# Performance work log

Measured on AMD Instinct MI355X. Metric: run time of the kernel, lower is better.

The kernel has to match this reference:

```python
import jax, jax.numpy as jnp
import numpy as np

INPUT_SIZE = 2048
HIDDEN_SIZE = 2048
BATCH = 4096


def setup_inputs() -> dict:
    key = jax.random.key(0)
    ks = jax.random.split(key, 16)
    s_in = 1.0 / np.sqrt(INPUT_SIZE)
    s_h = 1.0 / np.sqrt(HIDDEN_SIZE)
    d = {
        "x": jax.random.normal(ks[0], (BATCH, INPUT_SIZE), jnp.float32),
        "h": jax.random.normal(ks[1], (BATCH, HIDDEN_SIZE), jnp.float32),
        "c": jax.random.normal(ks[2], (BATCH, HIDDEN_SIZE), jnp.float32),
    }
    # input-side weights [H, I] and biases (torch nn.Linear layout)
    for i, g in enumerate(["f", "i", "c", "o"]):
        d[f"W{g}x"] = jax.random.uniform(ks[3 + i], (HIDDEN_SIZE, INPUT_SIZE), jnp.float32, -s_in, s_in)
        d[f"b{g}x"] = jax.random.uniform(ks[7 + i], (HIDDEN_SIZE,), jnp.float32, -s_in, s_in)
        d[f"W{g}h"] = jax.random.uniform(ks[11 + i], (HIDDEN_SIZE, HIDDEN_SIZE), jnp.float32, -s_h, s_h)
    return d


def reference(x, h, c, Wfx, bfx, Wfh, Wix, bix, Wih, Wcx, bcx, Wch, Wox, box, Woh):
    # gate pre-activations: x @ W*x.T + b + h @ W*h.T
    f = jax.nn.relu(x @ Wfx.T + bfx + h @ Wfh.T)
    i = jax.nn.relu(x @ Wix.T + bix + h @ Wih.T)
    o = jax.nn.relu(x @ Wox.T + box + h @ Woh.T)
    c_tilde = jnp.tanh(x @ Wcx.T + bcx + h @ Wch.T)
    c_new = f * c + i * c_tilde
    h_new = o * jnp.tanh(c_new)
    return (h_new, c_new)
```

## Files before the change

### kernel.cpp

```cpp
#include <hip/hip_runtime.h>
#include <hip/hip_bf16.h>


#define HID 2048
#define BATCH_N 4096
#define KTOT 4096
#define BK 64

typedef __attribute__((ext_vector_type(4))) float f32x4;
typedef __attribute__((ext_vector_type(8))) short bf16x8;

__device__ __forceinline__ short f2bf(float f) {
    union { float f; unsigned u; } v; v.f = f;
    unsigned r = v.u + 0x7FFFu + ((v.u >> 16) & 1u);
    return (short)(r >> 16);
}

__device__ __forceinline__ float fast_tanh(float v) {
    float e = __expf(2.0f * v);
    return 1.0f - 2.0f / (e + 1.0f);
}

__device__ __forceinline__ void gload_lds16(const short* g, short* l) {
    __builtin_amdgcn_global_load_lds(
        (const __attribute__((address_space(1))) unsigned int*)g,
        (__attribute__((address_space(3))) unsigned int*)l, 16, 0, 0);
}

struct CastParams {
    const float* x; const float* h;
    const float* Wx[4]; const float* Wh[4];
    short* A; short* B;
};

__global__ __launch_bounds__(256) void precast_kernel(CastParams q) {
    const long A_CH = (long)BATCH_N * (KTOT / 8);
    const long B_CH = 4L * HID * (KTOT / 8);
    const long total = A_CH + B_CH;
    for (long idx = (long)blockIdx.x * 256 + threadIdx.x; idx < total;
         idx += (long)gridDim.x * 256) {
        const float* src; short* dst; int row, k;
        if (idx < A_CH) {
            row = (int)(idx >> 9);
            k = (int)(idx & 511) << 3;
            src = (k < HID) ? &q.x[(size_t)row * HID + k]
                            : &q.h[(size_t)row * HID + (k - HID)];
            dst = &q.A[(size_t)row * KTOT];
        } else {
            long r = idx - A_CH;
            int g = (int)(r >> 20);
            int rem = (int)(r & ((1 << 20) - 1));
            row = rem >> 9;
            k = (rem & 511) << 3;
            src = (k < HID) ? &q.Wx[g][(size_t)row * HID + k]
                            : &q.Wh[g][(size_t)row * HID + (k - HID)];
            dst = &q.B[((size_t)g * HID + row) * KTOT];
        }
        float4 v0 = *(const float4*)src;
        float4 v1 = *(const float4*)(src + 4);
        int col = (k & ~63) | ((k & 63) ^ ((row & 7) << 3));
        bf16x8 s;
        s[0] = f2bf(v0.x); s[1] = f2bf(v0.y); s[2] = f2bf(v0.z); s[3] = f2bf(v0.w);
        s[4] = f2bf(v1.x); s[5] = f2bf(v1.y); s[6] = f2bf(v1.z); s[7] = f2bf(v1.w);
        *(bf16x8*)&dst[col] = s;
    }
}

struct GemmParams {
    const short* A; const short* B;
    const float* bx[4];
    const float* c;
    float* oh; float* oc;
};

__global__ __launch_bounds__(512, 2) void gemm_lstm_8ph(GemmParams p) {
    __shared__ short sA[2][16384];
    __shared__ short sB[2][16384];

    const int t = threadIdx.x;
    const int wave = t >> 6;
    const int lane = t & 63;
    const int wr = wave >> 1;
    const int wc = wave & 1;
    const int lr = lane & 15;
    const int lk = (lane >> 4) * 8;
    const int sw = (lane & 7) << 3;
    const int koff0 = lk ^ sw;
    const int koff1 = (32 + lk) ^ sw;

    const int bm = blockIdx.x * 256;
    const int bn = blockIdx.y * 64;

    const int aOff = (wr * 64 + lr) * 64;
    const int bOff = (wc * 32 + lr) * 64;

    const short* aSrc = p.A + (size_t)(bm + (t >> 3)) * KTOT + (t & 7) * 8;
    const short* bSrc = p.B + (size_t)(bn + (t >> 3)) * KTOT + (t & 7) * 8;
    const int ldsT = t * 8;

    f32x4 acc[4][4][2];
    #pragma unroll
    for (int g = 0; g < 4; ++g)
        #pragma unroll
        for (int m = 0; m < 4; ++m)
            #pragma unroll
            for (int n = 0; n < 2; ++n)
                acc[g][m][n] = (f32x4){0.f, 0.f, 0.f, 0.f};

    bf16x8 a[4][2];
    bf16x8 b[2][2];

#define STAGE_A(bf, u, kp) gload_lds16(aSrc + (size_t)(u) * 64 * KTOT + (kp), \
                                       &sA[bf][(u) * 4096 + ldsT])
#define STAGE_B(bf, g, kp) gload_lds16(bSrc + (size_t)(g) * HID * KTOT + (kp), \
                                       &sB[bf][(g) * 4096 + ldsT])
#define READ_A(bf) do { _Pragma("unroll") for (int m = 0; m < 4; ++m) { \
        a[m][0] = *(const bf16x8*)&sA[bf][aOff + m * 1024 + koff0]; \
        a[m][1] = *(const bf16x8*)&sA[bf][aOff + m * 1024 + koff1]; } } while (0)
#define READ_B(bf, g) do { _Pragma("unroll") for (int n = 0; n < 2; ++n) { \
        b[n][0] = *(const bf16x8*)&sB[bf][(g) * 4096 + bOff + n * 1024 + koff0]; \
        b[n][1] = *(const bf16x8*)&sB[bf][(g) * 4096 + bOff + n * 1024 + koff1]; } } while (0)
#define MFMA_G(g) do { __builtin_amdgcn_s_setprio(1); \
        _Pragma("unroll") for (int kk = 0; kk < 2; ++kk) \
        _Pragma("unroll") for (int n = 0; n < 2; ++n) \
        _Pragma("unroll") for (int m = 0; m < 4; ++m) \
            acc[g][m][n] = __builtin_amdgcn_mfma_f32_16x16x32_bf16( \
                a[m][kk], b[n][kk], acc[g][m][n], 0, 0, 0); \
        __builtin_amdgcn_s_setprio(0); } while (0)
#define BAR() __builtin_amdgcn_s_barrier()
#define VMCNT6() asm volatile("s_waitcnt vmcnt(6)" ::: "memory")

    STAGE_A(0, 0, 0); STAGE_A(0, 1, 0); STAGE_A(0, 2, 0); STAGE_A(0, 3, 0);
    STAGE_B(0, 0, 0); STAGE_B(0, 1, 0); STAGE_B(0, 2, 0); STAGE_B(0, 3, 0);
    STAGE_A(1, 0, BK); STAGE_A(1, 1, BK); STAGE_A(1, 2, BK); STAGE_A(1, 3, BK);
    STAGE_B(1, 0, BK); STAGE_B(1, 1, BK);
    VMCNT6();
    BAR();

    for (int it = 0; it < KTOT / (2 * BK); ++it) {
        const int kc1 = ((2 * it + 1) * BK) & (KTOT - 1);
        const int kc2 = ((2 * it + 2) * BK) & (KTOT - 1);
        const int kc3 = ((2 * it + 3) * BK) & (KTOT - 1);

        READ_A(0); READ_B(0, 0);
        STAGE_B(1, 2, kc1); STAGE_B(1, 3, kc1);
        BAR(); MFMA_G(0); BAR();
        READ_B(0, 1);
        STAGE_A(0, 0, kc2); STAGE_A(0, 1, kc2);
        BAR(); MFMA_G(1); BAR();
        READ_B(0, 2);
        STAGE_A(0, 2, kc2); STAGE_A(0, 3, kc2);
        BAR(); MFMA_G(2); BAR();
        READ_B(0, 3);
        STAGE_B(0, 0, kc2); STAGE_B(0, 1, kc2);
        VMCNT6();
        BAR(); MFMA_G(3); BAR();
        READ_A(1); READ_B(1, 0);
        STAGE_B(0, 2, kc2); STAGE_B(0, 3, kc2);
        BAR(); MFMA_G(0); BAR();
        READ_B(1, 1);
        STAGE_A(1, 0, kc3); STAGE_A(1, 1, kc3);
        BAR(); MFMA_G(1); BAR();
        READ_B(1, 2);
        STAGE_A(1, 2, kc3); STAGE_A(1, 3, kc3);
        BAR(); MFMA_G(2); BAR();
        READ_B(1, 3);
        STAGE_B(1, 0, kc3); STAGE_B(1, 1, kc3);
        VMCNT6();
        BAR(); MFMA_G(3); BAR();
    }
    asm volatile("s_waitcnt vmcnt(0)" ::: "memory");

    float bias[4][2];
    #pragma unroll
    for (int g = 0; g < 4; ++g)
        #pragma unroll
        for (int n = 0; n < 2; ++n)
            bias[g][n] = p.bx[g][bn + wc * 32 + n * 16 + lr];

    #pragma unroll
    for (int m = 0; m < 4; ++m) {
        int rbase = bm + wr * 64 + m * 16 + (lane >> 4) * 4;
        #pragma unroll
        for (int r = 0; r < 4; ++r) {
            int row = rbase + r;
            #pragma unroll
            for (int n = 0; n < 2; ++n) {
                int col = bn + wc * 32 + n * 16 + lr;
                float pf = acc[0][m][n][r] + bias[0][n];
                float pi = acc[1][m][n][r] + bias[1][n];
                float pc = acc[2][m][n][r] + bias[2][n];
                float po = acc[3][m][n][r] + bias[3][n];
                float fg = fmaxf(pf, 0.f);
                float ig = fmaxf(pi, 0.f);
                float og = fmaxf(po, 0.f);
                float ct = fast_tanh(pc);
                float cv = p.c[(size_t)row * HID + col];
                float cn = fg * cv + ig * ct;
                float hn = og * fast_tanh(cn);
                p.oh[(size_t)row * HID + col] = hn;
                p.oc[(size_t)row * HID + col] = cn;
            }
        }
    }
#undef STAGE_A
#undef STAGE_B
#undef READ_A
#undef READ_B
#undef MFMA_G
#undef BAR
#undef VMCNT6
}

struct Params {
    const float* x; const float* h; const float* c;
    const float* Wx[4]; const float* Wh[4]; const float* bx[4];
    float* oh; float* oc;
};

__global__ __launch_bounds__(256, 2) void relulstm_fallback(Params p) {
    __shared__ short sA[128 * 64];
    __shared__ short sB[4][64 * 64];
    const int t = threadIdx.x;
    const int bm = blockIdx.x * 128;
    const int bn = blockIdx.y * 64;
    const int wave = t >> 6;
    const int lane = t & 63;
    const int wm = (wave >> 1) * 64;
    const int wn = (wave & 1) * 32;
    const int lr = lane & 15;
    const int lk = (lane >> 4) * 8;

    f32x4 acc[4][4][2];
    #pragma unroll
    for (int g = 0; g < 4; ++g)
        #pragma unroll
        for (int m = 0; m < 4; ++m)
            #pragma unroll
            for (int n = 0; n < 2; ++n)
                acc[g][m][n] = (f32x4){0.f, 0.f, 0.f, 0.f};

    for (int k0 = 0; k0 < 2 * HID; k0 += BK) {
        const bool xpart = (k0 < HID);
        const int kb = k0 & (HID - 1);
        const float* __restrict__ srcA = xpart ? p.x : p.h;
        #pragma unroll
        for (int i2 = 0; i2 < 8; ++i2) {
            int cidx = t + i2 * 256;
            int row = cidx >> 4;
            int kc = cidx & 15;
            float4 v = *(const float4*)&srcA[(size_t)(bm + row) * HID + kb + kc * 4];
            int idx = row * BK + ((kc * 4) ^ ((row & 7) << 3));
            short4 s;
            s.x = f2bf(v.x); s.y = f2bf(v.y); s.z = f2bf(v.z); s.w = f2bf(v.w);
            *(short4*)&sA[idx] = s;
        }
        #pragma unroll
        for (int i2 = 0; i2 < 16; ++i2) {
            const int g = i2 >> 2;
            int rem = t + (i2 & 3) * 256;
            int row = rem >> 4;
            int kc = rem & 15;
            const float* __restrict__ srcB = xpart ? p.Wx[g] : p.Wh[g];
            float4 v = *(const float4*)&srcB[(size_t)(bn + row) * HID + kb + kc * 4];
            int idx = row * BK + ((kc * 4) ^ ((row & 7) << 3));
            short4 s;
            s.x = f2bf(v.x); s.y = f2bf(v.y); s.z = f2bf(v.z); s.w = f2bf(v.w);
            *(short4*)&sB[g][idx] = s;
        }
        __syncthreads();
        #pragma unroll
        for (int kk = 0; kk < 2; ++kk) {
            bf16x8 a[4];
            #pragma unroll
            for (int m = 0; m < 4; ++m) {
                int row = wm + m * 16 + lr;
                int kidx = (kk * 32 + lk) ^ ((row & 7) << 3);
                a[m] = *(const bf16x8*)&sA[row * BK + kidx];
            }
            #pragma unroll
            for (int g = 0; g < 4; ++g) {
                #pragma unroll
                for (int n = 0; n < 2; ++n) {
                    int brow = wn + n * 16 + lr;
                    int kidx = (kk * 32 + lk) ^ ((brow & 7) << 3);
                    bf16x8 b = *(const bf16x8*)&sB[g][brow * BK + kidx];
                    #pragma unroll
                    for (int m = 0; m < 4; ++m)
                        acc[g][m][n] = __builtin_amdgcn_mfma_f32_16x16x32_bf16(
                            a[m], b, acc[g][m][n], 0, 0, 0);
                }
            }
        }
        __syncthreads();
    }

    float bias[4][2];
    #pragma unroll
    for (int g = 0; g < 4; ++g)
        #pragma unroll
        for (int n = 0; n < 2; ++n)
            bias[g][n] = p.bx[g][bn + wn + n * 16 + lr];

    #pragma unroll
    for (int m = 0; m < 4; ++m) {
        int rbase = bm + wm + m * 16 + (lane >> 4) * 4;
        #pragma unroll
        for (int r = 0; r < 4; ++r) {
            int row = rbase + r;
            #pragma unroll
            for (int n = 0; n < 2; ++n) {
                int col = bn + wn + n * 16 + lr;
                float pf = acc[0][m][n][r] + bias[0][n];
                float pi = acc[1][m][n][r] + bias[1][n];
                float pc = acc[2][m][n][r] + bias[2][n];
                float po = acc[3][m][n][r] + bias[3][n];
                float fg = fmaxf(pf, 0.f);
                float ig = fmaxf(pi, 0.f);
                float og = fmaxf(po, 0.f);
                float ct = fast_tanh(pc);
                float cv = p.c[(size_t)row * HID + col];
                float cn = fg * cv + ig * ct;
                float hn = og * fast_tanh(cn);
                p.oh[(size_t)row * HID + col] = hn;
                p.oc[(size_t)row * HID + col] = cn;
            }
        }
    }
}

extern "C" void kernel_launch(void* const* d_in, const int* in_sizes, int n_in,
                              void* d_out, int out_size, void* d_ws, size_t ws_size,
                              hipStream_t stream) {
    (void)in_sizes; (void)n_in; (void)out_size;
    const size_t A_BYTES = (size_t)BATCH_N * KTOT * 2;
    const size_t B_BYTES = (size_t)4 * HID * KTOT * 2;

    if (ws_size >= A_BYTES + B_BYTES) {
        short* A = (short*)d_ws;
        short* B = A + (size_t)BATCH_N * KTOT;

        CastParams q;
        q.x = (const float*)d_in[0];
        q.h = (const float*)d_in[1];
        for (int g = 0; g < 4; ++g) {
            q.Wx[g] = (const float*)d_in[3 + 3 * g];
            q.Wh[g] = (const float*)d_in[5 + 3 * g];
        }
        q.A = A; q.B = B;
        precast_kernel<<<2048, 256, 0, stream>>>(q);

        GemmParams p;
        p.A = A; p.B = B;
        p.c = (const float*)d_in[2];
        for (int g = 0; g < 4; ++g) p.bx[g] = (const float*)d_in[4 + 3 * g];
        p.oh = (float*)d_out;
        p.oc = (float*)d_out + (size_t)BATCH_N * HID;
        dim3 grid(BATCH_N / 256, HID / 64);
        gemm_lstm_8ph<<<grid, 512, 0, stream>>>(p);
    } else {
        Params p;
        p.x = (const float*)d_in[0];
        p.h = (const float*)d_in[1];
        p.c = (const float*)d_in[2];
        for (int g = 0; g < 4; ++g) {
            p.Wx[g] = (const float*)d_in[3 + 3 * g];
            p.bx[g] = (const float*)d_in[4 + 3 * g];
            p.Wh[g] = (const float*)d_in[5 + 3 * g];
        }
        p.oh = (float*)d_out;
        p.oc = (float*)d_out + (size_t)BATCH_N * HID;
        dim3 grid(BATCH_N / 128, HID / 64);
        relulstm_fallback<<<grid, 256, 0, stream>>>(p);
    }
}
```

Measured before the change: 317.4 us.

## Switch to 32x32x16 MFMA tiles and remap blocks for L2 locality

Replaces the 16x16x32 bf16 MFMA tiling with 32x32x16 MFMAs, so each wave issues fewer, larger matrix instructions and issues fewer LDS reads per FLOP. The LDS fragment offsets and the fused LSTM epilogue's row/column mapping are rewritten to match the 32x32 accumulator layout. It also flattens the grid to 1D with an XCD-aware block swizzle to improve cache reuse, and adds an lgkmcnt wait before the first MFMA group. The changed epilogue store pattern and new wait placement could affect memory efficiency or overlap.

```diff
diff --git a/kernel.cpp b/kernel.cpp
--- a/kernel.cpp
+++ b/kernel.cpp
@@ -8,6 +8,7 @@
 #define BK 64
 
 typedef __attribute__((ext_vector_type(4))) float f32x4;
+typedef __attribute__((ext_vector_type(16))) float f32x16;
 typedef __attribute__((ext_vector_type(8))) short bf16x8;
 
 __device__ __forceinline__ short f2bf(float f) {
@@ -82,53 +83,56 @@
     const int lane = t & 63;
     const int wr = wave >> 1;
     const int wc = wave & 1;
-    const int lr = lane & 15;
-    const int lk = (lane >> 4) * 8;
-    const int sw = (lane & 7) << 3;
-    const int koff0 = lk ^ sw;
-    const int koff1 = (32 + lk) ^ sw;
-
-    const int bm = blockIdx.x * 256;
-    const int bn = blockIdx.y * 64;
-
-    const int aOff = (wr * 64 + lr) * 64;
-    const int bOff = (wc * 32 + lr) * 64;
+    const int l31 = lane & 31;
+    const int kb_ = (lane >> 5) * 8;
+    const int sw = (l31 & 7) << 3;
+
+    int kx[4];
+    #pragma unroll
+    for (int ks = 0; ks < 4; ++ks) kx[ks] = (ks * 16 + kb_) ^ sw;
+
+    const int b0 = blockIdx.x;
+    const int nb = ((b0 & 7) << 6) | (b0 >> 3);
+    const int bm = (nb & 15) * 256;
+    const int bn = (nb >> 4) * 64;
+
+    const int aOff = (wr * 64 + l31) * 64;
+    const int bOff = (wc * 32 + l31) * 64;
 
     const short* aSrc = p.A + (size_t)(bm + (t >> 3)) * KTOT + (t & 7) * 8;
     const short* bSrc = p.B + (size_t)(bn + (t >> 3)) * KTOT + (t & 7) * 8;
     const int ldsT = t * 8;
 
-    f32x4 acc[4][4][2];
+    f32x16 acc[4][2];
     #pragma unroll
     for (int g = 0; g < 4; ++g)
         #pragma unroll
-        for (int m = 0; m < 4; ++m)
-            #pragma unroll
-            for (int n = 0; n < 2; ++n)
-                acc[g][m][n] = (f32x4){0.f, 0.f, 0.f, 0.f};
-
-    bf16x8 a[4][2];
-    bf16x8 b[2][2];
+        for (int m = 0; m < 2; ++m)
+            #pragma unroll
+            for (int r = 0; r < 16; ++r)
+                acc[g][m][r] = 0.f;
+
+    bf16x8 a[2][4];
+    bf16x8 b[4];
 
 #define STAGE_A(bf, u, kp) gload_lds16(aSrc + (size_t)(u) * 64 * KTOT + (kp), \
                                        &sA[bf][(u) * 4096 + ldsT])
 #define STAGE_B(bf, g, kp) gload_lds16(bSrc + (size_t)(g) * HID * KTOT + (kp), \
                                        &sB[bf][(g) * 4096 + ldsT])
-#define READ_A(bf) do { _Pragma("unroll") for (int m = 0; m < 4; ++m) { \
-        a[m][0] = *(const bf16x8*)&sA[bf][aOff + m * 1024 + koff0]; \
-        a[m][1] = *(const bf16x8*)&sA[bf][aOff + m * 1024 + koff1]; } } while (0)
-#define READ_B(bf, g) do { _Pragma("unroll") for (int n = 0; n < 2; ++n) { \
-        b[n][0] = *(const bf16x8*)&sB[bf][(g) * 4096 + bOff + n * 1024 + koff0]; \
-        b[n][1] = *(const bf16x8*)&sB[bf][(g) * 4096 + bOff + n * 1024 + koff1]; } } while (0)
+#define READ_A(bf) do { _Pragma("unroll") for (int m = 0; m < 2; ++m) \
+        _Pragma("unroll") for (int ks = 0; ks < 4; ++ks) \
+            a[m][ks] = *(const bf16x8*)&sA[bf][aOff + m * 2048 + kx[ks]]; } while (0)
+#define READ_B(bf, g) do { _Pragma("unroll") for (int ks = 0; ks < 4; ++ks) \
+            b[ks] = *(const bf16x8*)&sB[bf][(g) * 4096 + bOff + kx[ks]]; } while (0)
 #define MFMA_G(g) do { __builtin_amdgcn_s_setprio(1); \
-        _Pragma("unroll") for (int kk = 0; kk < 2; ++kk) \
-        _Pragma("unroll") for (int n = 0; n < 2; ++n) \
-        _Pragma("unroll") for (int m = 0; m < 4; ++m) \
-            acc[g][m][n] = __builtin_amdgcn_mfma_f32_16x16x32_bf16( \
-                a[m][kk], b[n][kk], acc[g][m][n], 0, 0, 0); \
+        _Pragma("unroll") for (int ks = 0; ks < 4; ++ks) \
+        _Pragma("unroll") for (int m = 0; m < 2; ++m) \
+            acc[g][m] = __builtin_amdgcn_mfma_f32_32x32x16_bf16( \
+                a[m][ks], b[ks], acc[g][m], 0, 0, 0); \
         __builtin_amdgcn_s_setprio(0); } while (0)
 #define BAR() __builtin_amdgcn_s_barrier()
 #define VMCNT6() asm volatile("s_waitcnt vmcnt(6)" ::: "memory")
+#define LGKM8() asm volatile("s_waitcnt lgkmcnt(8)" ::: "memory")
 
     STAGE_A(0, 0, 0); STAGE_A(0, 1, 0); STAGE_A(0, 2, 0); STAGE_A(0, 3, 0);
     STAGE_B(0, 0, 0); STAGE_B(0, 1, 0); STAGE_B(0, 2, 0); STAGE_B(0, 3, 0);
@@ -144,6 +148,7 @@
 
         READ_A(0); READ_B(0, 0);
         STAGE_B(1, 2, kc1); STAGE_B(1, 3, kc1);
+        LGKM8();
         BAR(); MFMA_G(0); BAR();
         READ_B(0, 1);
         STAGE_A(0, 0, kc2); STAGE_A(0, 1, kc2);
@@ -157,6 +162,7 @@
         BAR(); MFMA_G(3); BAR();
         READ_A(1); READ_B(1, 0);
         STAGE_B(0, 2, kc2); STAGE_B(0, 3, kc2);
+        LGKM8();
         BAR(); MFMA_G(0); BAR();
         READ_B(1, 1);
         STAGE_A(1, 0, kc3); STAGE_A(1, 1, kc3);
@@ -171,36 +177,29 @@
     }
     asm volatile("s_waitcnt vmcnt(0)" ::: "memory");
 
-    float bias[4][2];
-    #pragma unroll
-    for (int g = 0; g < 4; ++g)
-        #pragma unroll
-        for (int n = 0; n < 2; ++n)
-            bias[g][n] = p.bx[g][bn + wc * 32 + n * 16 + lr];
-
-    #pragma unroll
-    for (int m = 0; m < 4; ++m) {
-        int rbase = bm + wr * 64 + m * 16 + (lane >> 4) * 4;
-        #pragma unroll
-        for (int r = 0; r < 4; ++r) {
-            int row = rbase + r;
-            #pragma unroll
-            for (int n = 0; n < 2; ++n) {
-                int col = bn + wc * 32 + n * 16 + lr;
-                float pf = acc[0][m][n][r] + bias[0][n];
-                float pi = acc[1][m][n][r] + bias[1][n];
-                float pc = acc[2][m][n][r] + bias[2][n];
-                float po = acc[3][m][n][r] + bias[3][n];
-                float fg = fmaxf(pf, 0.f);
-                float ig = fmaxf(pi, 0.f);
-                float og = fmaxf(po, 0.f);
-                float ct = fast_tanh(pc);
-                float cv = p.c[(size_t)row * HID + col];
-                float cn = fg * cv + ig * ct;
-                float hn = og * fast_tanh(cn);
-                p.oh[(size_t)row * HID + col] = hn;
-                p.oc[(size_t)row * HID + col] = cn;
-            }
+    const int col = bn + wc * 32 + l31;
+    float bias[4];
+    #pragma unroll
+    for (int g = 0; g < 4; ++g) bias[g] = p.bx[g][col];
+
+    #pragma unroll
+    for (int m = 0; m < 2; ++m) {
+        #pragma unroll
+        for (int r = 0; r < 16; ++r) {
+            int row = bm + wr * 64 + m * 32 + (r & 3) + 8 * (r >> 2) + 4 * (lane >> 5);
+            float pf = acc[0][m][r] + bias[0];
+            float pi = acc[1][m][r] + bias[1];
+            float pc = acc[2][m][r] + bias[2];
+            float po = acc[3][m][r] + bias[3];
+            float fg = fmaxf(pf, 0.f);
+            float ig = fmaxf(pi, 0.f);
+            float og = fmaxf(po, 0.f);
+            float ct = fast_tanh(pc);
+            float cv = p.c[(size_t)row * HID + col];
+            float cn = fg * cv + ig * ct;
+            float hn = og * fast_tanh(cn);
+            p.oh[(size_t)row * HID + col] = hn;
+            p.oc[(size_t)row * HID + col] = cn;
         }
     }
 #undef STAGE_A
@@ -210,6 +209,7 @@
 #undef MFMA_G
 #undef BAR
 #undef VMCNT6
+#undef LGKM8
 }
 
 struct Params {
@@ -356,8 +356,7 @@
         for (int g = 0; g < 4; ++g) p.bx[g] = (const float*)d_in[4 + 3 * g];
         p.oh = (float*)d_out;
         p.oc = (float*)d_out + (size_t)BATCH_N * HID;
-        dim3 grid(BATCH_N / 256, HID / 64);
-        gemm_lstm_8ph<<<grid, 512, 0, stream>>>(p);
+        gemm_lstm_8ph<<<dim3(512), 512, 0, stream>>>(p);
     } else {
         Params p;
         p.x = (const float*)d_in[0];
```

Result: slower. 352.2 us (+10.9%).

## Double-buffer LDS fragments in registers and halve barriers per GEMM phase

Applied to the files above, without the earlier changes.

Splits the A/B register fragments into two ping-pong sets, so the next gate's B fragment (and the next K-chunk's A fragment) is read from LDS while the current MFMA group runs. Each phase now ends with a single barrier plus a scheduling barrier instead of bracketing every MFMA group with two barriers. The vmcnt wait moves earlier and drops to 4, so the other buffer is complete before it is read ahead. This aims to hide LDS read latency and cut barrier stalls, at the cost of extra VGPRs for the second fragment set and a stricter scheduling order.

```diff
diff --git a/kernel.cpp b/kernel.cpp
--- a/kernel.cpp
+++ b/kernel.cpp
@@ -73,7 +73,7 @@
     float* oh; float* oc;
 };
 
-__global__ __launch_bounds__(512, 2) void gemm_lstm_8ph(GemmParams p) {
+__global__ __launch_bounds__(512, 2) void gemm_lstm_pipe(GemmParams p) {
     __shared__ short sA[2][16384];
     __shared__ short sB[2][16384];
 
@@ -107,67 +107,81 @@
             for (int n = 0; n < 2; ++n)
                 acc[g][m][n] = (f32x4){0.f, 0.f, 0.f, 0.f};
 
-    bf16x8 a[4][2];
-    bf16x8 b[2][2];
+    bf16x8 aX[4][2], aY[4][2];
+    bf16x8 bX[2][2], bY[2][2];
 
 #define STAGE_A(bf, u, kp) gload_lds16(aSrc + (size_t)(u) * 64 * KTOT + (kp), \
                                        &sA[bf][(u) * 4096 + ldsT])
 #define STAGE_B(bf, g, kp) gload_lds16(bSrc + (size_t)(g) * HID * KTOT + (kp), \
                                        &sB[bf][(g) * 4096 + ldsT])
-#define READ_A(bf) do { _Pragma("unroll") for (int m = 0; m < 4; ++m) { \
-        a[m][0] = *(const bf16x8*)&sA[bf][aOff + m * 1024 + koff0]; \
-        a[m][1] = *(const bf16x8*)&sA[bf][aOff + m * 1024 + koff1]; } } while (0)
-#define READ_B(bf, g) do { _Pragma("unroll") for (int n = 0; n < 2; ++n) { \
-        b[n][0] = *(const bf16x8*)&sB[bf][(g) * 4096 + bOff + n * 1024 + koff0]; \
-        b[n][1] = *(const bf16x8*)&sB[bf][(g) * 4096 + bOff + n * 1024 + koff1]; } } while (0)
-#define MFMA_G(g) do { __builtin_amdgcn_s_setprio(1); \
+#define READ_A_TO(dst, bf) do { _Pragma("unroll") for (int m = 0; m < 4; ++m) { \
+        dst[m][0] = *(const bf16x8*)&sA[bf][aOff + m * 1024 + koff0]; \
+        dst[m][1] = *(const bf16x8*)&sA[bf][aOff + m * 1024 + koff1]; } } while (0)
+#define READ_B_TO(dst, bf, g) do { _Pragma("unroll") for (int n = 0; n < 2; ++n) { \
+        dst[n][0] = *(const bf16x8*)&sB[bf][(g) * 4096 + bOff + n * 1024 + koff0]; \
+        dst[n][1] = *(const bf16x8*)&sB[bf][(g) * 4096 + bOff + n * 1024 + koff1]; } } while (0)
+#define MFMA_G(g, aS, bS) do { __builtin_amdgcn_s_setprio(1); \
         _Pragma("unroll") for (int kk = 0; kk < 2; ++kk) \
         _Pragma("unroll") for (int n = 0; n < 2; ++n) \
         _Pragma("unroll") for (int m = 0; m < 4; ++m) \
             acc[g][m][n] = __builtin_amdgcn_mfma_f32_16x16x32_bf16( \
-                a[m][kk], b[n][kk], acc[g][m][n], 0, 0, 0); \
+                aS[m][kk], bS[n][kk], acc[g][m][n], 0, 0, 0); \
         __builtin_amdgcn_s_setprio(0); } while (0)
-#define BAR() __builtin_amdgcn_s_barrier()
-#define VMCNT6() asm volatile("s_waitcnt vmcnt(6)" ::: "memory")
+#define ENDW() do { __builtin_amdgcn_s_barrier(); \
+                    __builtin_amdgcn_sched_barrier(0); } while (0)
+#define VMCNT(n) asm volatile("s_waitcnt vmcnt(" #n ")" ::: "memory")
 
     STAGE_A(0, 0, 0); STAGE_A(0, 1, 0); STAGE_A(0, 2, 0); STAGE_A(0, 3, 0);
     STAGE_B(0, 0, 0); STAGE_B(0, 1, 0); STAGE_B(0, 2, 0); STAGE_B(0, 3, 0);
     STAGE_A(1, 0, BK); STAGE_A(1, 1, BK); STAGE_A(1, 2, BK); STAGE_A(1, 3, BK);
     STAGE_B(1, 0, BK); STAGE_B(1, 1, BK);
-    VMCNT6();
-    BAR();
+    VMCNT(6);
+    __builtin_amdgcn_s_barrier();
+    READ_A_TO(aX, 0);
+    READ_B_TO(bX, 0, 0);
+    ENDW();
 
     for (int it = 0; it < KTOT / (2 * BK); ++it) {
         const int kc1 = ((2 * it + 1) * BK) & (KTOT - 1);
         const int kc2 = ((2 * it + 2) * BK) & (KTOT - 1);
         const int kc3 = ((2 * it + 3) * BK) & (KTOT - 1);
 
-        READ_A(0); READ_B(0, 0);
+        READ_B_TO(bY, 0, 1);
         STAGE_B(1, 2, kc1); STAGE_B(1, 3, kc1);
-        BAR(); MFMA_G(0); BAR();
-        READ_B(0, 1);
+        MFMA_G(0, aX, bX);
+        ENDW();
+        READ_B_TO(bX, 0, 2);
         STAGE_A(0, 0, kc2); STAGE_A(0, 1, kc2);
-        BAR(); MFMA_G(1); BAR();
-        READ_B(0, 2);
+        MFMA_G(1, aX, bY);
+        ENDW();
+        READ_B_TO(bY, 0, 3);
         STAGE_A(0, 2, kc2); STAGE_A(0, 3, kc2);
-        BAR(); MFMA_G(2); BAR();
-        READ_B(0, 3);
+        MFMA_G(2, aX, bX);
+        ENDW();
+        VMCNT(4);
+        READ_A_TO(aY, 1);
+        READ_B_TO(bX, 1, 0);
         STAGE_B(0, 0, kc2); STAGE_B(0, 1, kc2);
-        VMCNT6();
-        BAR(); MFMA_G(3); BAR();
-        READ_A(1); READ_B(1, 0);
+        MFMA_G(3, aX, bY);
+        ENDW();
+        READ_B_TO(bY, 1, 1);
         STAGE_B(0, 2, kc2); STAGE_B(0, 3, kc2);
-        BAR(); MFMA_G(0); BAR();
-        READ_B(1, 1);
+        MFMA_G(0, aY, bX);
+        ENDW();
+        READ_B_TO(bX, 1, 2);
         STAGE_A(1, 0, kc3); STAGE_A(1, 1, kc3);
-        BAR(); MFMA_G(1); BAR();
-        READ_B(1, 2);
+        MFMA_G(1, aY, bY);
+        ENDW();
+        READ_B_TO(bY, 1, 3);
         STAGE_A(1, 2, kc3); STAGE_A(1, 3, kc3);
-        BAR(); MFMA_G(2); BAR();
-        READ_B(1, 3);
+        MFMA_G(2, aY, bX);
+        ENDW();
+        VMCNT(4);
+        READ_A_TO(aX, 0);
+        READ_B_TO(bX, 0, 0);
         STAGE_B(1, 0, kc3); STAGE_B(1, 1, kc3);
-        VMCNT6();
-        BAR(); MFMA_G(3); BAR();
+        MFMA_G(3, aY, bY);
+        ENDW();
     }
     asm volatile("s_waitcnt vmcnt(0)" ::: "memory");
 
@@ -205,11 +219,11 @@
     }
 #undef STAGE_A
 #undef STAGE_B
-#undef READ_A
-#undef READ_B
+#undef READ_A_TO
+#undef READ_B_TO
 #undef MFMA_G
-#undef BAR
-#undef VMCNT6
+#undef ENDW
+#undef VMCNT
 }
 
 struct Params {
@@ -357,7 +371,7 @@
         p.oh = (float*)d_out;
         p.oc = (float*)d_out + (size_t)BATCH_N * HID;
         dim3 grid(BATCH_N / 256, HID / 64);
-        gemm_lstm_8ph<<<grid, 512, 0, stream>>>(p);
+        gemm_lstm_pipe<<<grid, 512, 0, stream>>>(p);
     } else {
         Params p;
         p.x = (const float*)d_in[0];
```

Measured after the change: 331.3 us. 4.4% more time.
